# Performance work log

Measured on AMD Instinct MI355X. Metric: run time of the kernel, lower is better.

Reference implementation:

```python
import jax, jax.numpy as jnp
import numpy as np

N_MET, N_RXN, N_GENE = 2534, 4881, 6607
E, P, D = 262144, 131072, 256
LN_EPS = 1e-5


def _segment_mean(x, idx, n):
    s = jax.ops.segment_sum(x, idx, num_segments=n)
    c = jax.ops.segment_sum(jnp.ones((idx.shape[0],), x.dtype), idx, num_segments=n)
    return s / jnp.maximum(c, 1.0)[:, None]


def _hyperconv(x, eattr, node, edge, stoich, W, We, att, b):
    # PyG-style HypergraphConv with stoichiometry as incidence weight + attention.
    xp = x @ W                      # [N_MET, D]
    ep = eattr @ We                 # [N_RXN, D]
    xi = xp[node]                   # [E, D] gather
    ej = ep[edge]                   # [E, D] gather
    logits = jax.nn.leaky_relu(jnp.concatenate([xi, ej], axis=-1) @ att, 0.2)  # [E]
    m = jax.ops.segment_max(logits, edge, num_segments=N_RXN)
    ex = jnp.exp(logits - m[edge])
    ssum = jax.ops.segment_sum(ex, edge, num_segments=N_RXN)
    alpha = ex / (ssum[edge] + 1e-16)           # softmax per hyperedge
    w = stoich * alpha                           # [E]
    ones = jnp.ones_like(stoich)
    Bc = jax.ops.segment_sum(ones, edge, num_segments=N_RXN)   # nodes per edge
    me = jax.ops.segment_sum(w[:, None] * xi, edge, num_segments=N_RXN)
    me = me / jnp.maximum(Bc, 1.0)[:, None]      # node -> hyperedge
    Dc = jax.ops.segment_sum(ones, node, num_segments=N_MET)   # edges per node
    out = jax.ops.segment_sum(w[:, None] * me[edge], node, num_segments=N_MET)
    out = out / jnp.maximum(Dc, 1.0)[:, None]    # hyperedge -> node
    return out + b


def _layernorm(z, g, b):
    mu = jnp.mean(z, axis=-1, keepdims=True)
    var = jnp.mean(jnp.square(z - mu), axis=-1, keepdims=True)
    return (z - mu) / jnp.sqrt(var + LN_EPS) * g + b


def _renorm(emb):
    # nn.Embedding(max_norm=1.0): clamp row norms to <= 1
    n = jnp.linalg.norm(emb, axis=-1, keepdims=True)
    return emb * jnp.minimum(1.0, 1.0 / (n + 1e-12))


def setup_inputs() -> dict:
    key = jax.random.key(0)
    ks = jax.random.split(key, 16)
    s = 1.0 / np.sqrt(D)
    return {
        "he_node": jax.random.randint(ks[0], (E,), 0, N_MET),
        "he_edge": jax.random.randint(ks[1], (E,), 0, N_RXN),
        "stoich": jax.random.normal(ks[2], (E,), dtype=jnp.float32),
        "gene_x": jax.random.normal(ks[3], (N_GENE, D), dtype=jnp.float32),
        "rtg_rxn": jax.random.randint(ks[4], (P,), 0, N_RXN),
        "rtg_gene": jax.random.randint(ks[5], (P,), 0, N_GENE),
        "emb_table": jax.random.normal(ks[6], (N_MET, D), dtype=jnp.float32) * 0.02,
        "W0": jax.random.normal(ks[7], (D, D), dtype=jnp.float32) * s,
        "We0": jax.random.normal(ks[8], (D, D), dtype=jnp.float32) * s,
        "att0": jax.random.normal(ks[9], (2 * D,), dtype=jnp.float32) * s,
        "b0": jnp.zeros((D,), jnp.float32),
        "W1": jax.random.normal(ks[10], (D, D), dtype=jnp.float32) * s,
        "We1": jax.random.normal(ks[11], (D, D), dtype=jnp.float32) * s,
        "att1": jax.random.normal(ks[12], (2 * D,), dtype=jnp.float32) * s,
        "b1": jnp.zeros((D,), jnp.float32),
        "ln_g": jnp.ones((D,), jnp.float32),
        "ln_b": jnp.zeros((D,), jnp.float32),
    }


def reference(he_node, he_edge, stoich, gene_x, rtg_rxn, rtg_gene, emb_table,
              W0, We0, att0, b0, W1, We1, att1, b1, ln_g, ln_b):
    met = _renorm(emb_table)                                    # [N_MET, D]
    # gene -> reaction scatter-mean (flattened reaction_to_genes dict)
    rxn_emb = _segment_mean(gene_x[rtg_gene], rtg_rxn, N_RXN)   # [N_RXN, D]
    # layer 0 (no skip on first layer)
    cur = jnp.tanh(_hyperconv(met, rxn_emb, he_node, he_edge, stoich, W0, We0, att0, b0))
    # layer 1 with skip + layernorm
    nxt = jnp.tanh(_hyperconv(cur, rxn_emb, he_node, he_edge, stoich, W1, We1, att1, b1))
    cur = _layernorm(nxt + cur, ln_g, ln_b)
    # metabolite -> reaction scatter-mean over incidences
    rxn_final = _segment_mean(cur[he_node], he_edge, N_RXN)     # [N_RXN, D]
    # reaction -> gene scatter-mean
    gene_emb = _segment_mean(rxn_final[rtg_rxn], rtg_gene, N_GENE)  # [N_GENE, D]
    return gene_emb
```

## Files before the change

kernel.cpp:

```cpp
#include <hip/hip_runtime.h>
#include <math.h>

#define DD 256
static constexpr int N_MET  = 2534;
static constexpr int N_RXN  = 4881;
static constexpr int N_GENE = 6607;
static constexpr int NE     = 262144;
static constexpr int NP     = 131072;

static constexpr int NCHUNK = 256;
static constexpr int NCHG   = 128;
static constexpr int NBE    = 77;
static constexpr int NBN    = 80;
static constexpr int NBG    = 104;
static constexpr int CHS    = 80;
static constexpr int GEMM_BLOCKS = (N_MET + 15) / 16;
static constexpr int KP2_GEMM0 = NBE + NBN + NBG;

__device__ __forceinline__ float waveSum(float v) {
  #pragma unroll
  for (int o = 32; o > 0; o >>= 1) v += __shfl_xor(v, o, 64);
  return v;
}
__device__ __forceinline__ float waveMax(float v) {
  #pragma unroll
  for (int o = 32; o > 0; o >>= 1) v = fmaxf(v, __shfl_xor(v, o, 64));
  return v;
}
__device__ __forceinline__ int   bcasti(int v, int l)   { return __builtin_amdgcn_readlane(v, l); }
__device__ __forceinline__ float bcastf(float v, int l) {
  return __int_as_float(__builtin_amdgcn_readlane(__float_as_int(v), l));
}

__global__ __launch_bounds__(1024) void KH_k(
    const int* __restrict__ he_node, const int* __restrict__ he_edge,
    const int* __restrict__ rtg_rxn, const int* __restrict__ rtg_gene,
    int* cntE, int* cntN, int* cntR, int* cntG,
    int* __restrict__ chE, int* __restrict__ chN, int* __restrict__ chG,
    const float* __restrict__ We0, const float* __restrict__ att0,
    const float* __restrict__ We1, const float* __restrict__ att1,
    float* __restrict__ ve0, float* __restrict__ ve1) {
  int blk = blockIdx.x, tid = threadIdx.x;
  if (blk < 32) {
    int wid = blk * 16 + (tid >> 6);
    int lane = tid & 63;
    const float* We = (wid < 256) ? We0 : We1;
    const float* at = (wid < 256) ? att0 : att1;
    int r = wid & 255;
    float4 a = ((const float4*)(We + (size_t)r * DD))[lane];
    float4 v = ((const float4*)(at + DD))[lane];
    float s = waveSum(a.x * v.x + a.y * v.y + a.z * v.z + a.w * v.w);
    if (lane == 0) ((wid < 256) ? ve0 : ve1)[r] = s;
    return;
  }
  int c = blk - 32;
  __shared__ int hE[NBE], hN[NBN], hG[NBG];
  if (tid < NBE) hE[tid] = 0;
  if (tid >= 128 && tid < 128 + NBN) hN[tid - 128] = 0;
  if (tid >= 256 && tid < 256 + NBG) hG[tid - 256] = 0;
  __syncthreads();
  int i = c * 1024 + tid;
  int n = he_node[i], e = he_edge[i];
  atomicAdd(&cntE[e], 1); atomicAdd(&cntN[n], 1);
  atomicAdd(&hE[e >> 6], 1); atomicAdd(&hN[n >> 5], 1);
  if (c < NCHG) {
    int r = rtg_rxn[i], g = rtg_gene[i];
    atomicAdd(&cntR[r], 1); atomicAdd(&cntG[g], 1);
    atomicAdd(&hG[g >> 6], 1);
  }
  __syncthreads();
  if (tid < NBE) chE[c * CHS + tid] = hE[tid];
  if (tid >= 128 && tid < 128 + NBN) chN[c * CHS + (tid - 128)] = hN[tid - 128];
  if (c < NCHG && tid >= 256 && tid < 256 + NBG) chG[c * NBG + (tid - 256)] = hG[tid - 256];
}

__global__ __launch_bounds__(1024) void KScan_k(
    const int* __restrict__ cntE, int* __restrict__ offsE,
    const int* __restrict__ cntN, int* __restrict__ offsN,
    const int* __restrict__ cntG, int* __restrict__ offsG,
    int* __restrict__ chE, int* __restrict__ chN, int* __restrict__ chG,
    const float* __restrict__ gene_x,
    const float* __restrict__ ve0, const float* __restrict__ ve1,
    float* __restrict__ gdot0, float* __restrict__ gdot1) {
  int blk = blockIdx.x, tid = threadIdx.x;
  if (blk < 3) {
    const int* cnt; int n; int* offs;
    if      (blk == 0) { cnt = cntE; n = N_RXN;  offs = offsE; }
    else if (blk == 1) { cnt = cntN; n = N_MET;  offs = offsN; }
    else               { cnt = cntG; n = N_GENE; offs = offsG; }
    __shared__ int part[1024];
    int base = tid * 8;
    int v[8]; int s = 0;
    #pragma unroll
    for (int j = 0; j < 8; ++j) { int x = (base + j < n) ? cnt[base + j] : 0; v[j] = x; s += x; }
    part[tid] = s;
    __syncthreads();
    for (int o = 1; o < 1024; o <<= 1) {
      int t = (tid >= o) ? part[tid - o] : 0;
      __syncthreads();
      part[tid] += t;
      __syncthreads();
    }
    int ex = part[tid] - s;
    #pragma unroll
    for (int j = 0; j < 8; ++j) {
      if (base + j < n) { offs[base + j] = ex; ex += v[j]; }
    }
    if (tid == 1023) offs[n] = part[1023];
    return;
  }
  if (blk < 20) {
    int colw = (blk - 3) * 16 + (tid >> 6);
    int lane = tid & 63;
    if (colw < NBE + NBN) {
      int side = colw >= NBE;
      int b = colw - side * NBE;
      int* ch = side ? chN : chE;
      int v[4]; int s = 0;
      int cbase = lane * 4;
      #pragma unroll
      for (int k = 0; k < 4; ++k) { v[k] = ch[(cbase + k) * CHS + b]; s += v[k]; }
      int inc = s;
      #pragma unroll
      for (int o = 1; o < 64; o <<= 1) { int t = __shfl_up(inc, o, 64); if (lane >= o) inc += t; }
      int ex = inc - s;
      #pragma unroll
      for (int k = 0; k < 4; ++k) { int t = v[k]; ch[(cbase + k) * CHS + b] = ex; ex += t; }
    } else if (colw < NBE + NBN + NBG) {
      int b = colw - NBE - NBN;
      int v[2]; int s = 0;
      int cbase = lane * 2;
      #pragma unroll
      for (int k = 0; k < 2; ++k) { v[k] = chG[(cbase + k) * NBG + b]; s += v[k]; }
      int inc = s;
      #pragma unroll
      for (int o = 1; o < 64; o <<= 1) { int t = __shfl_up(inc, o, 64); if (lane >= o) inc += t; }
      int ex = inc - s;
      #pragma unroll
      for (int k = 0; k < 2; ++k) { int t = v[k]; chG[(cbase + k) * NBG + b] = ex; ex += t; }
    }
    return;
  }
  int wid = (blk - 20) * 16 + (tid >> 6);
  int lane = tid & 63;
  if (wid >= N_GENE) return;
  float4 a  = ((const float4*)gene_x)[(size_t)wid * 64 + lane];
  float4 v0 = ((const float4*)ve0)[lane];
  float4 v1 = ((const float4*)ve1)[lane];
  float s0 = waveSum(a.x * v0.x + a.y * v0.y + a.z * v0.z + a.w * v0.w);
  float s1 = waveSum(a.x * v1.x + a.y * v1.y + a.z * v1.z + a.w * v1.w);
  if (lane == 0) { gdot0[wid] = s0; gdot1[wid] = s1; }
}

__global__ __launch_bounds__(1024) void KP1_k(
    const int* __restrict__ he_node, const int* __restrict__ he_edge,
    const float* __restrict__ stoich,
    const int* __restrict__ offsE, const int* __restrict__ offsN,
    const int* __restrict__ offsG,
    const int* __restrict__ chE, const int* __restrict__ chN,
    const int* __restrict__ chG,
    int4* __restrict__ scrE, int4* __restrict__ scrN, int2* __restrict__ scrG,
    const int* __restrict__ rtg_rxn, const int* __restrict__ rtg_gene,
    const float* __restrict__ gdot0, const float* __restrict__ gdot1,
    float* __restrict__ seAcc0, float* __restrict__ seAcc1) {
  int c = blockIdx.x, tid = threadIdx.x;
  __shared__ int cursE[NBE], cursN[NBN], cursG[NBG];
  if (tid < NBE) cursE[tid] = offsE[64 * tid] + chE[c * CHS + tid];
  if (tid >= 128 && tid < 128 + NBN) {
    int t = tid - 128;
    cursN[t] = offsN[32 * t] + chN[c * CHS + t];
  }
  if (c < NCHG && tid >= 256 && tid < 256 + NBG) {
    int t = tid - 256;
    cursG[t] = offsG[64 * t] + chG[c * NBG + t];
  }
  __syncthreads();
  int i = c * 1024 + tid;
  int n = he_node[i], e = he_edge[i];
  int st = __float_as_int(stoich[i]);
  int dE = atomicAdd(&cursE[e >> 6], 1);
  scrE[dE] = make_int4(e, n, st, 0);
  int dN = atomicAdd(&cursN[n >> 5], 1);
  scrN[dN] = make_int4(n, e, st, 0);
  if (c < NCHG) {
    int r = rtg_rxn[i], g = rtg_gene[i];
    int dG = atomicAdd(&cursG[g >> 6], 1);
    scrG[dG] = make_int2(g, r);
    atomicAdd(&seAcc0[r], gdot0[g]);
    atomicAdd(&seAcc1[r], gdot1[g]);
  }
}

template <bool RENORM>
__device__ __forceinline__ void gemm_body(const float* __restrict__ X,
                                          const float* __restrict__ W,
                                          const float* __restrict__ att,
                                          float* __restrict__ Y,
                                          float* __restrict__ sn, int M, int r0) {
  __shared__ float Xs[256][20];
  __shared__ float red[4][16];
  __shared__ float scl[16];
  int tid = threadIdx.x;
  int w = tid >> 6, lane = tid & 63;
  float xv[16];
  #pragma unroll
  for (int i = 0; i < 16; ++i) {
    int r = r0 + i;
    xv[i] = (r < M) ? X[(size_t)r * DD + tid] : 0.f;
  }
  if (RENORM) {
    #pragma unroll
    for (int i = 0; i < 16; ++i) {
      float v = waveSum(xv[i] * xv[i]);
      if (lane == 0) red[w][i] = v;
    }
    __syncthreads();
    if (tid < 16) {
      float t = red[0][tid] + red[1][tid] + red[2][tid] + red[3][tid];
      scl[tid] = fminf(1.f, 1.f / (sqrtf(t) + 1e-12f));
    }
    __syncthreads();
    #pragma unroll
    for (int i = 0; i < 16; ++i) xv[i] *= scl[i];
  }
  #pragma unroll
  for (int i = 0; i < 16; ++i) Xs[tid][i] = xv[i];
  __syncthreads();
  float acc[16];
  #pragma unroll
  for (int i = 0; i < 16; ++i) acc[i] = 0.f;
  const float* wp = W + tid;
  #pragma unroll 8
  for (int k = 0; k < 256; ++k) {
    float wv = wp[(size_t)k * DD];
    const float4* xr = reinterpret_cast<const float4*>(&Xs[k][0]);
    float4 a0 = xr[0], a1 = xr[1], a2 = xr[2], a3 = xr[3];
    acc[0]  += a0.x * wv; acc[1]  += a0.y * wv; acc[2]  += a0.z * wv; acc[3]  += a0.w * wv;
    acc[4]  += a1.x * wv; acc[5]  += a1.y * wv; acc[6]  += a1.z * wv; acc[7]  += a1.w * wv;
    acc[8]  += a2.x * wv; acc[9]  += a2.y * wv; acc[10] += a2.z * wv; acc[11] += a2.w * wv;
    acc[12] += a3.x * wv; acc[13] += a3.y * wv; acc[14] += a3.z * wv; acc[15] += a3.w * wv;
  }
  #pragma unroll
  for (int i = 0; i < 16; ++i) {
    int r = r0 + i;
    if (r < M) Y[(size_t)r * DD + tid] = acc[i];
  }
  float av = att[tid];
  __syncthreads();
  #pragma unroll
  for (int i = 0; i < 16; ++i) {
    float v = waveSum(acc[i] * av);
    if (lane == 0) red[w][i] = v;
  }
  __syncthreads();
  if (tid < 16) {
    int r = r0 + tid;
    if (r < M) sn[r] = red[0][tid] + red[1][tid] + red[2][tid] + red[3][tid];
  }
}

__global__ __launch_bounds__(256) void KP2_k(
    const int* __restrict__ offsE, const int* __restrict__ offsN,
    const int* __restrict__ offsG,
    const int4* __restrict__ scrE, const int4* __restrict__ scrN,
    const int2* __restrict__ scrG,
    int2* __restrict__ payE, int2* __restrict__ payN, int* __restrict__ rxnG,
    const float* __restrict__ emb, const float* __restrict__ W0,
    const float* __restrict__ att0, float* __restrict__ xp, float* __restrict__ sn) {
  int blk = blockIdx.x, tid = threadIdx.x;
  if (blk < NBE) {
    __shared__ int curs[64];
    int elo = 64 * blk;
    int ecnt = min(64, N_RXN - elo);
    if (tid < ecnt) curs[tid] = offsE[elo + tid];
    __syncthreads();
    int lo = offsE[elo], hi = offsE[elo + ecnt];
    for (int j = lo + tid; j < hi; j += 256) {
      int4 r = scrE[j];
      int slot = atomicAdd(&curs[r.x - elo], 1);
      payE[slot] = make_int2(r.y, r.z);
    }
  } else if (blk < NBE + NBN) {
    __shared__ int curs[32];
    int b = blk - NBE;
    int nlo = 32 * b;
    int ncnt = min(32, N_MET - nlo);
    if (tid < ncnt) curs[tid] = offsN[nlo + tid];
    __syncthreads();
    int lo = offsN[nlo], hi = offsN[nlo + ncnt];
    for (int j = lo + tid; j < hi; j += 256) {
      int4 r = scrN[j];
      int slot = atomicAdd(&curs[r.x - nlo], 1);
      payN[slot] = make_int2(r.y, r.z);
    }
  } else if (blk < KP2_GEMM0) {
    __shared__ int curs[64];
    int b = blk - NBE - NBN;
    int glo = 64 * b;
    int gcnt = min(64, N_GENE - glo);
    if (tid < gcnt) curs[tid] = offsG[glo + tid];
    __syncthreads();
    int lo = offsG[glo], hi = offsG[glo + gcnt];
    for (int j = lo + tid; j < hi; j += 256) {
      int2 r = scrG[j];
      int slot = atomicAdd(&curs[r.x - glo], 1);
      rxnG[slot] = r.y;
    }
  } else {
    gemm_body<true>(emb, W0, att0, xp, sn, N_MET, (blk - KP2_GEMM0) * 16);
  }
}

__global__ __launch_bounds__(256) void gemm1_k(const float* __restrict__ X,
                                               const float* __restrict__ W,
                                               const float* __restrict__ att,
                                               float* __restrict__ Y,
                                               float* __restrict__ sn, int M) {
  gemm_body<false>(X, W, att, Y, sn, M, blockIdx.x * 16);
}

__device__ __forceinline__ void gatherAcc(float4& acc, const float4* __restrict__ src4,
                                          const int (&rv)[4], const float (&wv)[4],
                                          int nc, int lane) {
  #pragma unroll
  for (int c = 0; c < 4; ++c) {
    int lim = nc - c * 64; if (lim > 64) lim = 64;
    for (int t = 0; t < lim; t += 16) {
      float4 a[16]; float w[16];
      #pragma unroll
      for (int q = 0; q < 16; ++q) {
        int   n = bcasti(rv[c], t + q);
        w[q]    = bcastf(wv[c], t + q);
        a[q]    = src4[(size_t)n * 64 + lane];
      }
      #pragma unroll
      for (int q = 0; q < 16; ++q) {
        acc.x += w[q] * a[q].x; acc.y += w[q] * a[q].y;
        acc.z += w[q] * a[q].z; acc.w += w[q] * a[q].w;
      }
    }
  }
}

template <int STRIDE>
__global__ __launch_bounds__(256) void seg_mean_k(const int* __restrict__ offs,
                                                  const int* __restrict__ pay,
                                                  const float* __restrict__ src,
                                                  float* __restrict__ dst, int nseg) {
  int wid = (blockIdx.x * 256 + threadIdx.x) >> 6;
  int lane = threadIdx.x & 63;
  if (wid >= nseg) return;
  int beg = offs[wid], end = offs[wid + 1];
  int cnt = end - beg;
  int nc = cnt < 256 ? cnt : 256;
  int rv[4]; float wv[4];
  #pragma unroll
  for (int c = 0; c < 4; ++c) {
    int j = c * 64 + lane;
    if (j < nc) { rv[c] = pay[(size_t)(beg + j) * STRIDE]; wv[c] = 1.f; }
    else        { rv[c] = 0;                               wv[c] = 0.f; }
  }
  float4 acc = make_float4(0.f, 0.f, 0.f, 0.f);
  gatherAcc(acc, (const float4*)src, rv, wv, nc, lane);
  for (int j = 256; j < cnt; ++j) {
    int n = pay[(size_t)(beg + j) * STRIDE];
    float4 a = ((const float4*)src)[(size_t)n * 64 + lane];
    acc.x += a.x; acc.y += a.y; acc.z += a.z; acc.w += a.w;
  }
  float inv = 1.f / (float)(cnt > 1 ? cnt : 1);
  float4 o; o.x = acc.x * inv; o.y = acc.y * inv; o.z = acc.z * inv; o.w = acc.w * inv;
  ((float4*)dst)[(size_t)wid * 64 + lane] = o;
}

__global__ __launch_bounds__(256) void me_k(const int* __restrict__ offs,
                                            const int2* __restrict__ payE,
                                            const float* __restrict__ sn,
                                            const float* __restrict__ seAcc,
                                            const int* __restrict__ cntR,
                                            const float* __restrict__ xp,
                                            float* __restrict__ me,
                                            float4* __restrict__ rstat) {
  int wid = (blockIdx.x * 256 + threadIdx.x) >> 6;
  int lane = threadIdx.x & 63;
  if (wid >= N_RXN) return;
  int rc = cntR[wid];
  float ser = seAcc[wid] / (float)(rc > 1 ? rc : 1);

  int beg = offs[wid], end = offs[wid + 1];
  int cnt = end - beg;
  int nc = cnt < 256 ? cnt : 256;
  int nv[4]; float wv[4]; float stv[4];
  float lmax = -1e30f;
  #pragma unroll
  for (int c = 0; c < 4; ++c) {
    int j = c * 64 + lane;
    if (j < nc) {
      int2 p = payE[beg + j];
      float l = sn[p.x] + ser;
      l = (l >= 0.f) ? l : 0.2f * l;
      nv[c] = p.x; wv[c] = l; stv[c] = __int_as_float(p.y);
      lmax = fmaxf(lmax, l);
    } else { nv[c] = 0; wv[c] = -1e30f; stv[c] = 0.f; }
  }
  for (int j = 256 + lane; j < cnt; j += 64) {
    int2 p = payE[beg + j];
    float l = sn[p.x] + ser;
    l = (l >= 0.f) ? l : 0.2f * l;
    lmax = fmaxf(lmax, l);
  }
  float m = waveMax(lmax);
  float s = 0.f;
  #pragma unroll
  for (int c = 0; c < 4; ++c) {
    if (c * 64 + lane < nc) { float e = expf(wv[c] - m); wv[c] = e; s += e; }
    else wv[c] = 0.f;
  }
  for (int j = 256 + lane; j < cnt; j += 64) {
    int2 p = payE[beg + j];
    float l = sn[p.x] + ser;
    l = (l >= 0.f) ? l : 0.2f * l;
    s += expf(l - m);
  }
  s = waveSum(s);
  float invS = 1.f / (s + 1e-16f);
  #pragma unroll
  for (int c = 0; c < 4; ++c) {
    if (c * 64 + lane < nc) wv[c] = stv[c] * wv[c] * invS;
  }
  if (lane == 0) rstat[wid] = make_float4(ser, m, invS, 0.f);
  float4 acc = make_float4(0.f, 0.f, 0.f, 0.f);
  gatherAcc(acc, (const float4*)xp, nv, wv, nc, lane);
  for (int j = 256; j < cnt; ++j) {
    int2 p = payE[beg + j];
    float l = sn[p.x] + ser;
    l = (l >= 0.f) ? l : 0.2f * l;
    float w = __int_as_float(p.y) * expf(l - m) * invS;
    float4 a = ((const float4*)xp)[(size_t)p.x * 64 + lane];
    acc.x += w * a.x; acc.y += w * a.y; acc.z += w * a.z; acc.w += w * a.w;
  }
  float invB = 1.f / (float)(cnt > 1 ? cnt : 1);
  float4 o; o.x = acc.x * invB; o.y = acc.y * invB; o.z = acc.z * invB; o.w = acc.w * invB;
  ((float4*)me)[(size_t)wid * 64 + lane] = o;
}

template <bool LN>
__global__ __launch_bounds__(256) void out_k(const int* __restrict__ offs,
                                             const int2* __restrict__ payN,
                                             const float* __restrict__ sn,
                                             const float4* __restrict__ rstat,
                                             const float* __restrict__ me,
                                             const float* __restrict__ bias,
                                             const float* __restrict__ ln_g,
                                             const float* __restrict__ ln_b,
                                             float* __restrict__ cur) {
  int wid = (blockIdx.x * 256 + threadIdx.x) >> 6;
  int lane = threadIdx.x & 63;
  if (wid >= N_MET) return;
  int beg = offs[wid], end = offs[wid + 1];
  int cnt = end - beg;
  int nc = cnt < 256 ? cnt : 256;
  float sn_n = sn[wid];
  int rv[4]; float wv[4];
  #pragma unroll
  for (int c = 0; c < 4; ++c) {
    int j = c * 64 + lane;
    if (j < nc) {
      int2 p = payN[beg + j];
      float4 st = rstat[p.x];
      float l = sn_n + st.x;
      l = (l >= 0.f) ? l : 0.2f * l;
      rv[c] = p.x;
      wv[c] = __int_as_float(p.y) * expf(l - st.y) * st.z;
    } else { rv[c] = 0; wv[c] = 0.f; }
  }
  float4 acc = make_float4(0.f, 0.f, 0.f, 0.f);
  gatherAcc(acc, (const float4*)me, rv, wv, nc, lane);
  for (int j = 256; j < cnt; ++j) {
    int2 p = payN[beg + j];
    float4 st = rstat[p.x];
    float l = sn_n + st.x;
    l = (l >= 0.f) ? l : 0.2f * l;
    float w = __int_as_float(p.y) * expf(l - st.y) * st.z;
    float4 a = ((const float4*)me)[(size_t)p.x * 64 + lane];
    acc.x += w * a.x; acc.y += w * a.y; acc.z += w * a.z; acc.w += w * a.w;
  }
  float invD = 1.f / (float)(cnt > 1 ? cnt : 1);
  float4 b4 = ((const float4*)bias)[lane];
  float4 o;
  o.x = tanhf(acc.x * invD + b4.x);
  o.y = tanhf(acc.y * invD + b4.y);
  o.z = tanhf(acc.z * invD + b4.z);
  o.w = tanhf(acc.w * invD + b4.w);
  float4* cur4 = (float4*)cur;
  if (!LN) {
    cur4[(size_t)wid * 64 + lane] = o;
    return;
  }
  float4 p = cur4[(size_t)wid * 64 + lane];
  float4 z; z.x = o.x + p.x; z.y = o.y + p.y; z.z = o.z + p.z; z.w = o.w + p.w;
  float mu = waveSum(z.x + z.y + z.z + z.w) * (1.f / 256.f);
  float4 zc; zc.x = z.x - mu; zc.y = z.y - mu; zc.z = z.z - mu; zc.w = z.w - mu;
  float var = waveSum(zc.x * zc.x + zc.y * zc.y + zc.z * zc.z + zc.w * zc.w) * (1.f / 256.f);
  float rs = 1.f / sqrtf(var + 1e-5f);
  float4 g4 = ((const float4*)ln_g)[lane];
  float4 be4 = ((const float4*)ln_b)[lane];
  float4 r;
  r.x = zc.x * rs * g4.x + be4.x;
  r.y = zc.y * rs * g4.y + be4.y;
  r.z = zc.z * rs * g4.z + be4.z;
  r.w = zc.w * rs * g4.w + be4.w;
  cur4[(size_t)wid * 64 + lane] = r;
}

extern "C" void kernel_launch(void* const* d_in, const int* in_sizes, int n_in,
                              void* d_out, int out_size, void* d_ws, size_t ws_size,
                              hipStream_t stream) {
  const int*   he_node = (const int*)d_in[0];
  const int*   he_edge = (const int*)d_in[1];
  const float* stoich  = (const float*)d_in[2];
  const float* gene_x  = (const float*)d_in[3];
  const int*   rtg_rxn = (const int*)d_in[4];
  const int*   rtg_gene= (const int*)d_in[5];
  const float* emb     = (const float*)d_in[6];
  const float* W0      = (const float*)d_in[7];
  const float* We0     = (const float*)d_in[8];
  const float* att0    = (const float*)d_in[9];
  const float* b0      = (const float*)d_in[10];
  const float* W1      = (const float*)d_in[11];
  const float* We1     = (const float*)d_in[12];
  const float* att1    = (const float*)d_in[13];
  const float* b1      = (const float*)d_in[14];
  const float* ln_g    = (const float*)d_in[15];
  const float* ln_b    = (const float*)d_in[16];
  float* out = (float*)d_out;

  char* base = (char*)d_ws;
  size_t off = 0;
  auto carve = [&](size_t bytes) -> char* {
    char* p = base + off;
    off += (bytes + 255) & ~(size_t)255;
    return p;
  };
  float*  xp    = (float*)carve((size_t)N_MET * DD * 4);
  float*  me    = (float*)carve((size_t)N_RXN * DD * 4);
  float*  cur   = (float*)carve((size_t)N_MET * DD * 4);
  float*  rxnf  = (float*)carve((size_t)N_RXN * DD * 4);
  float*  sn    = (float*)carve((size_t)N_MET * 4);
  float*  ve0   = (float*)carve(DD * 4);
  float*  ve1   = (float*)carve(DD * 4);
  float*  gdot0 = (float*)carve((size_t)N_GENE * 4);
  float*  gdot1 = (float*)carve((size_t)N_GENE * 4);
  float4* rstat = (float4*)carve((size_t)N_RXN * 16);
  int ztot = N_RXN + N_MET + N_RXN + N_GENE + 2 * N_RXN;
  int* zbase = (int*)carve((size_t)ztot * 4);
  int*   cntE   = zbase;
  int*   cntN   = cntE + N_RXN;
  int*   cntR   = cntN + N_MET;
  int*   cntG   = cntR + N_RXN;
  float* seAcc0 = (float*)(cntG + N_GENE);
  float* seAcc1 = seAcc0 + N_RXN;
  int*  offsE = (int*)carve((N_RXN + 1) * 4);
  int2* payE  = (int2*)carve((size_t)NE * 8);
  int*  offsN = (int*)carve((N_MET + 1) * 4);
  int2* payN  = (int2*)carve((size_t)NE * 8);
  int*  offsG = (int*)carve((N_GENE + 1) * 4);
  int*  rxnG  = (int*)carve((size_t)NP * 4);
  int4* scrE  = (int4*)carve((size_t)NE * 16);
  int4* scrN  = (int4*)carve((size_t)NE * 16);
  int2* scrG  = (int2*)carve((size_t)NP * 8);
  int*  chE   = (int*)carve((size_t)NCHUNK * CHS * 4);
  int*  chN   = (int*)carve((size_t)NCHUNK * CHS * 4);
  int*  chG   = (int*)carve((size_t)NCHG * NBG * 4);

  hipMemsetAsync(zbase, 0, (size_t)ztot * 4, stream);

  KH_k<<<32 + NCHUNK, 1024, 0, stream>>>(
      he_node, he_edge, rtg_rxn, rtg_gene, cntE, cntN, cntR, cntG,
      chE, chN, chG, We0, att0, We1, att1, ve0, ve1);

  int gdot_blocks = (N_GENE + 15) / 16;
  KScan_k<<<20 + gdot_blocks, 1024, 0, stream>>>(
      cntE, offsE, cntN, offsN, cntG, offsG,
      chE, chN, chG, gene_x, ve0, ve1, gdot0, gdot1);

  KP1_k<<<NCHUNK, 1024, 0, stream>>>(
      he_node, he_edge, stoich, offsE, offsN, offsG, chE, chN, chG,
      scrE, scrN, scrG, rtg_rxn, rtg_gene, gdot0, gdot1, seAcc0, seAcc1);

  KP2_k<<<KP2_GEMM0 + GEMM_BLOCKS, 256, 0, stream>>>(
      offsE, offsN, offsG, scrE, scrN, scrG, payE, payN, rxnG,
      emb, W0, att0, xp, sn);

  me_k<<<(N_RXN + 3) / 4, 256, 0, stream>>>(offsE, payE, sn, seAcc0, cntR,
                                            xp, me, rstat);
  out_k<false><<<(N_MET + 3) / 4, 256, 0, stream>>>(offsN, payN, sn, rstat, me, b0,
                                                    nullptr, nullptr, cur);

  gemm1_k<<<GEMM_BLOCKS, 256, 0, stream>>>(cur, W1, att1, xp, sn, N_MET);
  me_k<<<(N_RXN + 3) / 4, 256, 0, stream>>>(offsE, payE, sn, seAcc1, cntR,
                                            xp, me, rstat);
  out_k<true><<<(N_MET + 3) / 4, 256, 0, stream>>>(offsN, payN, sn, rstat, me, b1,
                                                   ln_g, ln_b, cur);

  seg_mean_k<2><<<(N_RXN + 3) / 4, 256, 0, stream>>>(offsE, (const int*)payE, cur, rxnf, N_RXN);
  seg_mean_k<1><<<(N_GENE + 3) / 4, 256, 0, stream>>>(offsG, rxnG, rxnf, out, N_GENE);
}
```

Measured before the change: 229.1 us.

## Drop global per-key count atomics, derive offsets in partition pass, split me_k

Removes the global per-key atomic counters and the single-block exclusive scans for edge, node and gene offsets. Per-bucket totals are now produced by the chunk scan and prefix-summed in LDS inside KP1, and KP2 builds the final per-key offsets by counting keys within each bucket. Scratch records are bit-packed (int4 to int2, int2 to int) to cut scatter bandwidth. me_k is split so two waves handle each reaction, each covering half the feature columns as float2. The cost is an extra counting pass in KP2 and duplicated softmax-statistics work in me_k.

```diff
diff --git a/kernel.cpp b/kernel.cpp
--- a/kernel.cpp
+++ b/kernel.cpp
@@ -14,6 +14,7 @@
 static constexpr int NBN    = 80;
 static constexpr int NBG    = 104;
 static constexpr int CHS    = 80;
+static constexpr int NCOL   = NBE + NBN + NBG;
 static constexpr int GEMM_BLOCKS = (N_MET + 15) / 16;
 static constexpr int KP2_GEMM0 = NBE + NBN + NBG;
 
@@ -35,7 +36,7 @@
 __global__ __launch_bounds__(1024) void KH_k(
     const int* __restrict__ he_node, const int* __restrict__ he_edge,
     const int* __restrict__ rtg_rxn, const int* __restrict__ rtg_gene,
-    int* cntE, int* cntN, int* cntR, int* cntG,
+    int* cntR,
     int* __restrict__ chE, int* __restrict__ chN, int* __restrict__ chG,
     const float* __restrict__ We0, const float* __restrict__ att0,
     const float* __restrict__ We1, const float* __restrict__ att1,
@@ -61,11 +62,10 @@
   __syncthreads();
   int i = c * 1024 + tid;
   int n = he_node[i], e = he_edge[i];
-  atomicAdd(&cntE[e], 1); atomicAdd(&cntN[n], 1);
   atomicAdd(&hE[e >> 6], 1); atomicAdd(&hN[n >> 5], 1);
   if (c < NCHG) {
     int r = rtg_rxn[i], g = rtg_gene[i];
-    atomicAdd(&cntR[r], 1); atomicAdd(&cntG[g], 1);
+    atomicAdd(&cntR[r], 1);
     atomicAdd(&hG[g >> 6], 1);
   }
   __syncthreads();
@@ -75,47 +75,21 @@
 }
 
 __global__ __launch_bounds__(1024) void KScan_k(
-    const int* __restrict__ cntE, int* __restrict__ offsE,
-    const int* __restrict__ cntN, int* __restrict__ offsN,
-    const int* __restrict__ cntG, int* __restrict__ offsG,
     int* __restrict__ chE, int* __restrict__ chN, int* __restrict__ chG,
+    int* __restrict__ totE, int* __restrict__ totN, int* __restrict__ totG,
     const float* __restrict__ gene_x,
     const float* __restrict__ ve0, const float* __restrict__ ve1,
     float* __restrict__ gdot0, float* __restrict__ gdot1) {
   int blk = blockIdx.x, tid = threadIdx.x;
-  if (blk < 3) {
-    const int* cnt; int n; int* offs;
-    if      (blk == 0) { cnt = cntE; n = N_RXN;  offs = offsE; }
-    else if (blk == 1) { cnt = cntN; n = N_MET;  offs = offsN; }
-    else               { cnt = cntG; n = N_GENE; offs = offsG; }
-    __shared__ int part[1024];
-    int base = tid * 8;
-    int v[8]; int s = 0;
-    #pragma unroll
-    for (int j = 0; j < 8; ++j) { int x = (base + j < n) ? cnt[base + j] : 0; v[j] = x; s += x; }
-    part[tid] = s;
-    __syncthreads();
-    for (int o = 1; o < 1024; o <<= 1) {
-      int t = (tid >= o) ? part[tid - o] : 0;
-      __syncthreads();
-      part[tid] += t;
-      __syncthreads();
-    }
-    int ex = part[tid] - s;
-    #pragma unroll
-    for (int j = 0; j < 8; ++j) {
-      if (base + j < n) { offs[base + j] = ex; ex += v[j]; }
-    }
-    if (tid == 1023) offs[n] = part[1023];
-    return;
-  }
-  if (blk < 20) {
-    int colw = (blk - 3) * 16 + (tid >> 6);
+  if (blk < 17) {
+    int colw = blk * 16 + (tid >> 6);
     int lane = tid & 63;
+    if (colw >= NCOL) return;
     if (colw < NBE + NBN) {
       int side = colw >= NBE;
       int b = colw - side * NBE;
       int* ch = side ? chN : chE;
+      int* tot = side ? totN : totE;
       int v[4]; int s = 0;
       int cbase = lane * 4;
       #pragma unroll
@@ -123,10 +97,11 @@
       int inc = s;
       #pragma unroll
       for (int o = 1; o < 64; o <<= 1) { int t = __shfl_up(inc, o, 64); if (lane >= o) inc += t; }
+      if (lane == 63) tot[b] = inc;
       int ex = inc - s;
       #pragma unroll
       for (int k = 0; k < 4; ++k) { int t = v[k]; ch[(cbase + k) * CHS + b] = ex; ex += t; }
-    } else if (colw < NBE + NBN + NBG) {
+    } else {
       int b = colw - NBE - NBN;
       int v[2]; int s = 0;
       int cbase = lane * 2;
@@ -135,13 +110,14 @@
       int inc = s;
       #pragma unroll
       for (int o = 1; o < 64; o <<= 1) { int t = __shfl_up(inc, o, 64); if (lane >= o) inc += t; }
+      if (lane == 63) totG[b] = inc;
       int ex = inc - s;
       #pragma unroll
       for (int k = 0; k < 2; ++k) { int t = v[k]; chG[(cbase + k) * NBG + b] = ex; ex += t; }
     }
     return;
   }
-  int wid = (blk - 20) * 16 + (tid >> 6);
+  int wid = (blk - 17) * 16 + (tid >> 6);
   int lane = tid & 63;
   if (wid >= N_GENE) return;
   float4 a  = ((const float4*)gene_x)[(size_t)wid * 64 + lane];
@@ -152,40 +128,62 @@
   if (lane == 0) { gdot0[wid] = s0; gdot1[wid] = s1; }
 }
 
+__device__ __forceinline__ void ldsScan128(int* sc, int tid) {
+  #pragma unroll
+  for (int o = 1; o < 128; o <<= 1) {
+    int t = (tid < 128 && tid >= o) ? sc[tid - o] : 0;
+    __syncthreads();
+    if (tid < 128) sc[tid] += t;
+    __syncthreads();
+  }
+}
+
 __global__ __launch_bounds__(1024) void KP1_k(
     const int* __restrict__ he_node, const int* __restrict__ he_edge,
     const float* __restrict__ stoich,
-    const int* __restrict__ offsE, const int* __restrict__ offsN,
-    const int* __restrict__ offsG,
     const int* __restrict__ chE, const int* __restrict__ chN,
     const int* __restrict__ chG,
-    int4* __restrict__ scrE, int4* __restrict__ scrN, int2* __restrict__ scrG,
+    const int* __restrict__ totE, const int* __restrict__ totN,
+    const int* __restrict__ totG,
+    int2* __restrict__ scrE, int2* __restrict__ scrN, int* __restrict__ scrG,
     const int* __restrict__ rtg_rxn, const int* __restrict__ rtg_gene,
     const float* __restrict__ gdot0, const float* __restrict__ gdot1,
     float* __restrict__ seAcc0, float* __restrict__ seAcc1) {
   int c = blockIdx.x, tid = threadIdx.x;
+  __shared__ int sc[128];
   __shared__ int cursE[NBE], cursN[NBN], cursG[NBG];
-  if (tid < NBE) cursE[tid] = offsE[64 * tid] + chE[c * CHS + tid];
-  if (tid >= 128 && tid < 128 + NBN) {
-    int t = tid - 128;
-    cursN[t] = offsN[32 * t] + chN[c * CHS + t];
-  }
-  if (c < NCHG && tid >= 256 && tid < 256 + NBG) {
-    int t = tid - 256;
-    cursG[t] = offsG[64 * t] + chG[c * NBG + t];
+  int v;
+  if (tid < 128) sc[tid] = (tid < NBE) ? totE[tid] : 0;
+  if (tid < 128) v = sc[tid];
+  __syncthreads();
+  ldsScan128(sc, tid);
+  if (tid < NBE) cursE[tid] = (sc[tid] - v) + chE[c * CHS + tid];
+  __syncthreads();
+  if (tid < 128) sc[tid] = (tid < NBN) ? totN[tid] : 0;
+  if (tid < 128) v = sc[tid];
+  __syncthreads();
+  ldsScan128(sc, tid);
+  if (tid < NBN) cursN[tid] = (sc[tid] - v) + chN[c * CHS + tid];
+  __syncthreads();
+  if (c < NCHG) {
+    if (tid < 128) sc[tid] = (tid < NBG) ? totG[tid] : 0;
+    if (tid < 128) v = sc[tid];
+    __syncthreads();
+    ldsScan128(sc, tid);
+    if (tid < NBG) cursG[tid] = (sc[tid] - v) + chG[c * NBG + tid];
   }
   __syncthreads();
   int i = c * 1024 + tid;
   int n = he_node[i], e = he_edge[i];
   int st = __float_as_int(stoich[i]);
   int dE = atomicAdd(&cursE[e >> 6], 1);
-  scrE[dE] = make_int4(e, n, st, 0);
+  scrE[dE] = make_int2((e << 12) | n, st);
   int dN = atomicAdd(&cursN[n >> 5], 1);
-  scrN[dN] = make_int4(n, e, st, 0);
+  scrN[dN] = make_int2((n << 13) | e, st);
   if (c < NCHG) {
     int r = rtg_rxn[i], g = rtg_gene[i];
     int dG = atomicAdd(&cursG[g >> 6], 1);
-    scrG[dG] = make_int2(g, r);
+    scrG[dG] = (g << 13) | r;
     atomicAdd(&seAcc0[r], gdot0[g]);
     atomicAdd(&seAcc1[r], gdot1[g]);
   }
@@ -259,55 +257,79 @@
   }
 }
 
+__device__ __forceinline__ int blockSumInt256(int v) {
+  __shared__ int s4[4];
+  #pragma unroll
+  for (int o = 32; o > 0; o >>= 1) v += __shfl_xor(v, o, 64);
+  if ((threadIdx.x & 63) == 0) s4[threadIdx.x >> 6] = v;
+  __syncthreads();
+  return s4[0] + s4[1] + s4[2] + s4[3];
+}
+
 __global__ __launch_bounds__(256) void KP2_k(
-    const int* __restrict__ offsE, const int* __restrict__ offsN,
-    const int* __restrict__ offsG,
-    const int4* __restrict__ scrE, const int4* __restrict__ scrN,
-    const int2* __restrict__ scrG,
+    const int* __restrict__ totE, const int* __restrict__ totN,
+    const int* __restrict__ totG,
+    const int2* __restrict__ scrE, const int2* __restrict__ scrN,
+    const int* __restrict__ scrG,
+    int* __restrict__ offsE, int* __restrict__ offsN, int* __restrict__ offsG,
     int2* __restrict__ payE, int2* __restrict__ payN, int* __restrict__ rxnG,
     const float* __restrict__ emb, const float* __restrict__ W0,
     const float* __restrict__ att0, float* __restrict__ xp, float* __restrict__ sn) {
   int blk = blockIdx.x, tid = threadIdx.x;
-  if (blk < NBE) {
-    __shared__ int curs[64];
-    int elo = 64 * blk;
-    int ecnt = min(64, N_RXN - elo);
-    if (tid < ecnt) curs[tid] = offsE[elo + tid];
-    __syncthreads();
-    int lo = offsE[elo], hi = offsE[elo + ecnt];
-    for (int j = lo + tid; j < hi; j += 256) {
-      int4 r = scrE[j];
-      int slot = atomicAdd(&curs[r.x - elo], 1);
-      payE[slot] = make_int2(r.y, r.z);
+  if (blk >= KP2_GEMM0) {
+    gemm_body<true>(emb, W0, att0, xp, sn, N_MET, (blk - KP2_GEMM0) * 16);
+    return;
+  }
+  __shared__ int cnt[64];
+  __shared__ int curs[64];
+  int side, b, klo, kcnt, nk, btot;
+  const int* tot;
+  if (blk < NBE)            { side = 0; b = blk;             tot = totE; klo = 64 * b; nk = N_RXN;  kcnt = min(64, N_RXN  - klo); }
+  else if (blk < NBE + NBN) { side = 1; b = blk - NBE;       tot = totN; klo = 32 * b; nk = N_MET;  kcnt = min(32, N_MET  - klo); }
+  else                      { side = 2; b = blk - NBE - NBN; tot = totG; klo = 64 * b; nk = N_GENE; kcnt = min(64, N_GENE - klo); }
+  btot = tot[b];
+  int pv = (tid < b) ? tot[tid] : 0;
+  int base = blockSumInt256(pv);
+  if (tid < 64) cnt[tid] = 0;
+  __syncthreads();
+  int lo = base, hi = base + btot;
+  for (int j = lo + tid; j < hi; j += 256) {
+    int key;
+    if (side == 0)      key = (scrE[j].x >> 12) - klo;
+    else if (side == 1) key = (scrN[j].x >> 13) - klo;
+    else                key = (scrG[j]   >> 13) - klo;
+    atomicAdd(&cnt[key], 1);
+  }
+  __syncthreads();
+  if (tid < 64) {
+    int v = cnt[tid];
+    int inc = v;
+    #pragma unroll
+    for (int o = 1; o < 64; o <<= 1) { int t = __shfl_up(inc, o, 64); if (tid >= o) inc += t; }
+    int ex = inc - v;
+    curs[tid] = base + ex;
+    int* offs = (side == 0) ? offsE : (side == 1) ? offsN : offsG;
+    if (tid < kcnt) offs[klo + tid] = base + ex;
+    if (tid == 0 && klo + kcnt == nk) offs[nk] = base + btot;
+  }
+  __syncthreads();
+  for (int j = lo + tid; j < hi; j += 256) {
+    if (side == 0) {
+      int2 r = scrE[j];
+      int e = r.x >> 12, n = r.x & 4095;
+      int slot = atomicAdd(&curs[e - klo], 1);
+      payE[slot] = make_int2(n, r.y);
+    } else if (side == 1) {
+      int2 r = scrN[j];
+      int n = r.x >> 13, e = r.x & 8191;
+      int slot = atomicAdd(&curs[n - klo], 1);
+      payN[slot] = make_int2(e, r.y);
+    } else {
+      int pw = scrG[j];
+      int g = pw >> 13, rr = pw & 8191;
+      int slot = atomicAdd(&curs[g - klo], 1);
+      rxnG[slot] = rr;
     }
-  } else if (blk < NBE + NBN) {
-    __shared__ int curs[32];
-    int b = blk - NBE;
-    int nlo = 32 * b;
-    int ncnt = min(32, N_MET - nlo);
-    if (tid < ncnt) curs[tid] = offsN[nlo + tid];
-    __syncthreads();
-    int lo = offsN[nlo], hi = offsN[nlo + ncnt];
-    for (int j = lo + tid; j < hi; j += 256) {
-      int4 r = scrN[j];
-      int slot = atomicAdd(&curs[r.x - nlo], 1);
-      payN[slot] = make_int2(r.y, r.z);
-    }
-  } else if (blk < KP2_GEMM0) {
-    __shared__ int curs[64];
-    int b = blk - NBE - NBN;
-    int glo = 64 * b;
-    int gcnt = min(64, N_GENE - glo);
-    if (tid < gcnt) curs[tid] = offsG[glo + tid];
-    __syncthreads();
-    int lo = offsG[glo], hi = offsG[glo + gcnt];
-    for (int j = lo + tid; j < hi; j += 256) {
-      int2 r = scrG[j];
-      int slot = atomicAdd(&curs[r.x - glo], 1);
-      rxnG[slot] = r.y;
-    }
-  } else {
-    gemm_body<true>(emb, W0, att0, xp, sn, N_MET, (blk - KP2_GEMM0) * 16);
   }
 }
 
@@ -337,6 +359,28 @@
       for (int q = 0; q < 16; ++q) {
         acc.x += w[q] * a[q].x; acc.y += w[q] * a[q].y;
         acc.z += w[q] * a[q].z; acc.w += w[q] * a[q].w;
+      }
+    }
+  }
+}
+
+__device__ __forceinline__ void gatherAcc2(float2& acc, const float2* __restrict__ src2,
+                                           const int (&rv)[4], const float (&wv)[4],
+                                           int nc, int fbase) {
+  #pragma unroll
+  for (int c = 0; c < 4; ++c) {
+    int lim = nc - c * 64; if (lim > 64) lim = 64;
+    for (int t = 0; t < lim; t += 16) {
+      float2 a[16]; float w[16];
+      #pragma unroll
+      for (int q = 0; q < 16; ++q) {
+        int   n = bcasti(rv[c], t + q);
+        w[q]    = bcastf(wv[c], t + q);
+        a[q]    = src2[(size_t)n * 128 + fbase];
+      }
+      #pragma unroll
+      for (int q = 0; q < 16; ++q) {
+        acc.x += w[q] * a[q].x; acc.y += w[q] * a[q].y;
       }
     }
   }
@@ -380,7 +424,8 @@
                                             const float* __restrict__ xp,
                                             float* __restrict__ me,
                                             float4* __restrict__ rstat) {
-  int wid = (blockIdx.x * 256 + threadIdx.x) >> 6;
+  int gw = (blockIdx.x * 256 + threadIdx.x) >> 6;
+  int wid = gw >> 1, half = gw & 1;
   int lane = threadIdx.x & 63;
   if (wid >= N_RXN) return;
   int rc = cntR[wid];
@@ -427,20 +472,21 @@
   for (int c = 0; c < 4; ++c) {
     if (c * 64 + lane < nc) wv[c] = stv[c] * wv[c] * invS;
   }
-  if (lane == 0) rstat[wid] = make_float4(ser, m, invS, 0.f);
-  float4 acc = make_float4(0.f, 0.f, 0.f, 0.f);
-  gatherAcc(acc, (const float4*)xp, nv, wv, nc, lane);
+  if (half == 0 && lane == 0) rstat[wid] = make_float4(ser, m, invS, 0.f);
+  int fbase = half * 64 + lane;
+  float2 acc = make_float2(0.f, 0.f);
+  gatherAcc2(acc, (const float2*)xp, nv, wv, nc, fbase);
   for (int j = 256; j < cnt; ++j) {
     int2 p = payE[beg + j];
     float l = sn[p.x] + ser;
     l = (l >= 0.f) ? l : 0.2f * l;
     float w = __int_as_float(p.y) * expf(l - m) * invS;
-    float4 a = ((const float4*)xp)[(size_t)p.x * 64 + lane];
-    acc.x += w * a.x; acc.y += w * a.y; acc.z += w * a.z; acc.w += w * a.w;
+    float2 a = ((const float2*)xp)[(size_t)p.x * 128 + fbase];
+    acc.x += w * a.x; acc.y += w * a.y;
   }
   float invB = 1.f / (float)(cnt > 1 ? cnt : 1);
-  float4 o; o.x = acc.x * invB; o.y = acc.y * invB; o.z = acc.z * invB; o.w = acc.w * invB;
-  ((float4*)me)[(size_t)wid * 64 + lane] = o;
+  float2 o; o.x = acc.x * invB; o.y = acc.y * invB;
+  ((float2*)me)[(size_t)wid * 128 + fbase] = o;
 }
 
 template <bool LN>
@@ -551,13 +597,10 @@
   float*  gdot0 = (float*)carve((size_t)N_GENE * 4);
   float*  gdot1 = (float*)carve((size_t)N_GENE * 4);
   float4* rstat = (float4*)carve((size_t)N_RXN * 16);
-  int ztot = N_RXN + N_MET + N_RXN + N_GENE + 2 * N_RXN;
+  int ztot = 3 * N_RXN;
   int* zbase = (int*)carve((size_t)ztot * 4);
-  int*   cntE   = zbase;
-  int*   cntN   = cntE + N_RXN;
-  int*   cntR   = cntN + N_MET;
-  int*   cntG   = cntR + N_RXN;
-  float* seAcc0 = (float*)(cntG + N_GENE);
+  int*   cntR   = zbase;
+  float* seAcc0 = (float*)(cntR + N_RXN);
   float* seAcc1 = seAcc0 + N_RXN;
   int*  offsE = (int*)carve((N_RXN + 1) * 4);
   int2* payE  = (int2*)carve((size_t)NE * 8);
@@ -565,40 +608,43 @@
   int2* payN  = (int2*)carve((size_t)NE * 8);
   int*  offsG = (int*)carve((N_GENE + 1) * 4);
   int*  rxnG  = (int*)carve((size_t)NP * 4);
-  int4* scrE  = (int4*)carve((size_t)NE * 16);
-  int4* scrN  = (int4*)carve((size_t)NE * 16);
-  int2* scrG  = (int2*)carve((size_t)NP * 8);
+  int2* scrE  = (int2*)carve((size_t)NE * 8);
+  int2* scrN  = (int2*)carve((size_t)NE * 8);
+  int*  scrG  = (int*)carve((size_t)NP * 4);
   int*  chE   = (int*)carve((size_t)NCHUNK * CHS * 4);
   int*  chN   = (int*)carve((size_t)NCHUNK * CHS * 4);
   int*  chG   = (int*)carve((size_t)NCHG * NBG * 4);
+  int*  totE  = (int*)carve(128 * 4);
+  int*  totN  = (int*)carve(128 * 4);
+  int*  totG  = (int*)carve(128 * 4);
 
   hipMemsetAsync(zbase, 0, (size_t)ztot * 4, stream);
 
   KH_k<<<32 + NCHUNK, 1024, 0, stream>>>(
-      he_node, he_edge, rtg_rxn, rtg_gene, cntE, cntN, cntR, cntG,
+      he_node, he_edge, rtg_rxn, rtg_gene, cntR,
       chE, chN, chG, We0, att0, We1, att1, ve0, ve1);
 
   int gdot_blocks = (N_GENE + 15) / 16;
-  KScan_k<<<20 + gdot_blocks, 1024, 0, stream>>>(
-      cntE, offsE, cntN, offsN, cntG, offsG,
-      chE, chN, chG, gene_x, ve0, ve1, gdot0, gdot1);
+  KScan_k<<<17 + gdot_blocks, 1024, 0, stream>>>(
+      chE, chN, chG, totE, totN, totG, gene_x, ve0, ve1, gdot0, gdot1);
 
   KP1_k<<<NCHUNK, 1024, 0, stream>>>(
-      he_node, he_edge, stoich, offsE, offsN, offsG, chE, chN, chG,
+      he_node, he_edge, stoich, chE, chN, chG, totE, totN, totG,
       scrE, scrN, scrG, rtg_rxn, rtg_gene, gdot0, gdot1, seAcc0, seAcc1);
 
   KP2_k<<<KP2_GEMM0 + GEMM_BLOCKS, 256, 0, stream>>>(
-      offsE, offsN, offsG, scrE, scrN, scrG, payE, payN, rxnG,
+      totE, totN, totG, scrE, scrN, scrG,
+      offsE, offsN, offsG, payE, payN, rxnG,
       emb, W0, att0, xp, sn);
 
-  me_k<<<(N_RXN + 3) / 4, 256, 0, stream>>>(offsE, payE, sn, seAcc0, cntR,
-                                            xp, me, rstat);
+  me_k<<<(2 * N_RXN + 3) / 4, 256, 0, stream>>>(offsE, payE, sn, seAcc0, cntR,
+                                                xp, me, rstat);
   out_k<false><<<(N_MET + 3) / 4, 256, 0, stream>>>(offsN, payN, sn, rstat, me, b0,
                                                     nullptr, nullptr, cur);
 
   gemm1_k<<<GEMM_BLOCKS, 256, 0, stream>>>(cur, W1, att1, xp, sn, N_MET);
-  me_k<<<(N_RXN + 3) / 4, 256, 0, stream>>>(offsE, payE, sn, seAcc1, cntR,
-                                            xp, me, rstat);
+  me_k<<<(2 * N_RXN + 3) / 4, 256, 0, stream>>>(offsE, payE, sn, seAcc1, cntR,
+                                                xp, me, rstat);
   out_k<true><<<(N_MET + 3) / 4, 256, 0, stream>>>(offsN, payN, sn, rstat, me, b1,
                                                    ln_g, ln_b, cur);
 
```

New measurement: 221.8 us. -3.2%, faster.
